# Kernel tuning notes

Measured on AMD Instinct MI355X. Metric: run time of the kernel, lower is better.

The kernel has to match this reference:

```python
import jax, jax.numpy as jnp
import numpy as np
from jax import lax

DIM = 384
HEADS = 8
H = W = 32
N = H * W
B = 8
FH, FW = 32, 17  # rfft2 spectral dims: H, W//2+1
EPS = 1e-5


def setup_inputs() -> dict:
    key = jax.random.key(0)
    ks = jax.random.split(key, 24)
    g = lambda i, shape, s=0.02: jax.random.normal(ks[i], shape, dtype=jnp.float32) * s
    inp = {
        "x": jax.random.normal(ks[0], (B, N, DIM), dtype=jnp.float32),
        "cw": g(1, (DIM, FH, FW, 2)),               # complex spectral weight
        # depthwise conv weights (C,1,3,3), kaiming-like std sqrt(2/(9))
        "dwq": jax.random.normal(ks[2], (DIM, 1, 3, 3), dtype=jnp.float32) * np.sqrt(2.0 / 9.0),
        "dwk": jax.random.normal(ks[3], (DIM, 1, 3, 3), dtype=jnp.float32) * np.sqrt(2.0 / 9.0),
        "dwv": jax.random.normal(ks[4], (DIM, 1, 3, 3), dtype=jnp.float32) * np.sqrt(2.0 / 9.0),
        # batchnorm params (inference mode)
        "gq": jnp.ones((DIM,), jnp.float32), "bq": jnp.zeros((DIM,), jnp.float32),
        "mq": g(5, (DIM,), 0.1), "vq": jnp.abs(g(6, (DIM,), 0.1)) + 1.0,
        "gk": jnp.ones((DIM,), jnp.float32), "bk": jnp.zeros((DIM,), jnp.float32),
        "mk": g(7, (DIM,), 0.1), "vk": jnp.abs(g(8, (DIM,), 0.1)) + 1.0,
        "gv": jnp.ones((DIM,), jnp.float32), "bv": jnp.zeros((DIM,), jnp.float32),
        "mv": g(9, (DIM,), 0.1), "vv": jnp.abs(g(10, (DIM,), 0.1)) + 1.0,
        # linear projections (torch Linear weight layout: (out,in), y = x @ W.T)
        "wq": g(11, (DIM, DIM)), "wk": g(12, (DIM, DIM)), "wv": g(13, (DIM, DIM)),
        "wo": g(14, (DIM, DIM)), "bo": jnp.zeros((DIM,), jnp.float32),
    }
    return inp


def _dw_bn(y, w, gamma, beta, mean, var):
    # depthwise 3x3 conv (stride 1, pad 1, no bias) + inference BN -> (B, N, C)
    y = lax.conv_general_dilated(
        y, w, window_strides=(1, 1), padding=[(1, 1), (1, 1)],
        dimension_numbers=("NCHW", "OIHW", "NCHW"), feature_group_count=DIM)
    scale = (gamma / jnp.sqrt(var + EPS))[None, :, None, None]
    shift = (beta - mean * gamma / jnp.sqrt(var + EPS))[None, :, None, None]
    y = y * scale + shift
    return y.reshape(y.shape[0], DIM, -1).transpose(0, 2, 1)  # b (h w) c


def reference(x, cw, dwq, dwk, dwv, gq, bq, mq, vq, gk, bk, mk, vk,
              gv, bv, mv, vv, wq, wk, wv, wo, bo):
    Bc, Nc, C = x.shape
    # --- F3Filter (flag='Learn'): FFT2 -> complex weight -> iFFT2 ---
    xi = x.reshape(Bc, H, W, C).transpose(0, 3, 1, 2)            # B,C,H,W
    xf = jnp.fft.rfft2(xi, axes=(2, 3), norm="ortho")            # B,C,H,W//2+1
    weight = cw[..., 0] + 1j * cw[..., 1]                        # C,FH,FW
    xr = jnp.fft.irfft2(xf * weight, s=(H, W), axes=(2, 3), norm="ortho")
    x_fft = xr.reshape(Bc, C, Nc).transpose(0, 2, 1)             # B,N,C

    # --- conv QKV projections on x_fft (as B,C,H,W = xr) ---
    q = _dw_bn(xr, dwq, gq, bq, mq, vq)
    k = _dw_bn(xr, dwk, gk, bk, mk, vk)
    v = _dw_bn(xr, dwv, gv, bv, mv, vv)

    hd = C // HEADS
    def split_heads(t):
        return t.reshape(Bc, Nc, HEADS, hd).transpose(0, 2, 1, 3)  # b h t d
    q = split_heads(q @ wq.T)
    k = split_heads(k @ wk.T)
    v = split_heads(v @ wv.T)

    scale = C ** (-0.5)  # note: full dim, as in the original
    attn = jax.nn.softmax(jnp.einsum("bhld,bhtd->bhlt", q, k) * scale, axis=-1)
    out = jnp.einsum("bhlt,bhtd->bhld", attn, v)
    out = out.transpose(0, 2, 1, 3).reshape(Bc, Nc, C)
    out = out @ wo.T + bo
    return x_fft + out
```

## Files before the change

kernel.cpp:

```cpp
#include <hip/hip_runtime.h>
#include <hip/hip_bf16.h>
#include <cmath>

#define CDIM 384
#define NB 8
#define NPIX 1024

typedef __attribute__((ext_vector_type(8))) short short8v;
typedef __attribute__((ext_vector_type(4))) float float4v;

__device__ __forceinline__ ushort f2bf(float f) {
  union { float f; unsigned u; } v; v.f = f;
  unsigned r = (v.u + 0x7fffu + ((v.u >> 16) & 1u)) >> 16;
  return (ushort)r;
}
__device__ __forceinline__ float bf2f(ushort u) {
  union { unsigned u; float f; } v; v.u = ((unsigned)u) << 16;
  return v.f;
}

__global__ __launch_bounds__(256) void prep_k(
    ushort* __restrict__ tbl,
    const float* __restrict__ wq, const float* __restrict__ wk,
    const float* __restrict__ wv, const float* __restrict__ wo,
    ushort* __restrict__ wqb, ushort* __restrict__ wkb,
    ushort* __restrict__ wvb, ushort* __restrict__ wob,
    const float* __restrict__ x, ushort* __restrict__ xc)
{
  __shared__ ushort T[128][33];
  if (blockIdx.x < 20) {
    int i = blockIdx.x * 256 + threadIdx.x;
    if (i >= 5 * 1024) return;
    int t = i >> 10, j = i & 1023, r = j >> 5, cidx = j & 31;
    float ang = (float)((r * cidx) & 31) * 0.19634954084936207f;
    float val;
    if (t == 0) val = cosf(ang);
    else if (t == 1) val = sinf(ang);
    else if (t == 2) val = -sinf(ang);
    else {
      if (cidx > 16) val = 0.f;
      else {
        float cv = (cidx == 0 || cidx == 16) ? 1.f : 2.f;
        val = (t == 3) ? cv * cosf(ang) : -cv * sinf(ang);
      }
    }
    tbl[i] = f2bf(val);
  } else if (blockIdx.x < 164) {
    int i = (blockIdx.x - 20) * 256 + threadIdx.x;
    if (i * 4 >= CDIM * CDIM) return;
    float4 va = *(const float4*)&wq[i * 4];
    float4 vb = *(const float4*)&wk[i * 4];
    float4 vc = *(const float4*)&wv[i * 4];
    float4 vd = *(const float4*)&wo[i * 4];
    ushort4 ra = { f2bf(va.x), f2bf(va.y), f2bf(va.z), f2bf(va.w) };
    ushort4 rb = { f2bf(vb.x), f2bf(vb.y), f2bf(vb.z), f2bf(vb.w) };
    ushort4 rc = { f2bf(vc.x), f2bf(vc.y), f2bf(vc.z), f2bf(vc.w) };
    ushort4 rd = { f2bf(vd.x), f2bf(vd.y), f2bf(vd.z), f2bf(vd.w) };
    *(ushort4*)&wqb[i * 4] = ra;
    *(ushort4*)&wkb[i * 4] = rb;
    *(ushort4*)&wvb[i * 4] = rc;
    *(ushort4*)&wob[i * 4] = rd;
  } else {
    int t = blockIdx.x - 164;
    int b = t / 96, rr = t % 96;
    int c0 = (rr >> 3) * 32, n0 = (rr & 7) * 128;
    for (int i = threadIdx.x; i < 4096; i += 256) {
      int n = i >> 5, c = i & 31;
      T[n][c] = f2bf(x[((long)(b * 1024 + n0 + n)) * CDIM + c0 + c]);
    }
    __syncthreads();
    for (int i = threadIdx.x; i < 4096; i += 256) {
      int c = i >> 7, n = i & 127;
      xc[((long)(b * CDIM + c0 + c)) * 1024 + n0 + n] = T[n][c];
    }
  }
}

__global__ __launch_bounds__(256) void fft_conv_k(
    const ushort* __restrict__ xc, const float* __restrict__ cw,
    const ushort* __restrict__ tbl,
    const float* __restrict__ dwq, const float* __restrict__ dwk, const float* __restrict__ dwv,
    const float* __restrict__ gq, const float* __restrict__ bq, const float* __restrict__ mq, const float* __restrict__ vq,
    const float* __restrict__ gk, const float* __restrict__ bk, const float* __restrict__ mk, const float* __restrict__ vk,
    const float* __restrict__ gv, const float* __restrict__ bv, const float* __restrict__ mv, const float* __restrict__ vv,
    ushort* __restrict__ yc,
    ushort* __restrict__ qc, ushort* __restrict__ kc, ushort* __restrict__ vc)
{
  const int b = blockIdx.x / CDIM, c = blockIdx.x % CDIM;
  const int tid = threadIdx.x;
  const int w = tid >> 6, lane = tid & 63;
  const int l15 = lane & 15, l16 = lane >> 4;
  __shared__ ushort B[11][32][40];
  __shared__ float Ysf[32][33];

  float wq9[9], wk9[9], wv9[9];
#pragma unroll
  for (int t = 0; t < 9; ++t) {
    wq9[t] = dwq[c * 9 + t];
    wk9[t] = dwk[c * 9 + t];
    wv9[t] = dwv[c * 9 + t];
  }
  float scq = gq[c] * rsqrtf(vq[c] + 1e-5f); float shq = bq[c] - mq[c] * scq;
  float sck = gk[c] * rsqrtf(vk[c] + 1e-5f); float shk = bk[c] - mk[c] * sck;
  float scv = gv[c] * rsqrtf(vv[c] + 1e-5f); float shv = bv[c] - mv[c] * scv;

  for (int i = tid; i < 640; i += 256) {
    int t = i >> 7, j = i & 127, r = j >> 2, s = j & 3;
    *(uint4*)&B[t][r][s * 8] = *(const uint4*)&tbl[t * 1024 + r * 32 + s * 8];
  }
  for (int i = tid; i < 1024; i += 256)
    B[5][i & 31][i >> 5] = xc[(long)(b * CDIM + c) * 1024 + i];
  __syncthreads();

  for (int j = w; j < 8; j += 4) {
    int o = j & 1, ut = (j >> 1) & 1, wt = (j >> 2) & 1;
    short8v af = *(const short8v*)&B[o == 0 ? 0 : 2][ut * 16 + l15][l16 * 8];
    short8v bf = *(const short8v*)&B[5][wt * 16 + l15][l16 * 8];
    float4v acc = {0.f, 0.f, 0.f, 0.f};
    acc = __builtin_amdgcn_mfma_f32_16x16x32_bf16(af, bf, acc, 0, 0, 0);
    int dst = (o == 0) ? 7 : 8;
#pragma unroll
    for (int r = 0; r < 4; ++r)
      B[dst][ut * 16 + l16 * 4 + r][wt * 16 + l15] = f2bf(acc[r]);
  }
  __syncthreads();

  for (int j = w; j < 8; j += 4) {
    int o = j & 1, ut = (j >> 1) & 1, vt = (j >> 2) & 1;
    short8v a1 = *(const short8v*)&B[o == 0 ? 7 : 8][ut * 16 + l15][l16 * 8];
    short8v b1 = *(const short8v*)&B[0][vt * 16 + l15][l16 * 8];
    short8v a2 = *(const short8v*)&B[o == 0 ? 8 : 7][ut * 16 + l15][l16 * 8];
    short8v b2 = *(const short8v*)&B[o == 0 ? 1 : 2][vt * 16 + l15][l16 * 8];
    float4v acc = {0.f, 0.f, 0.f, 0.f};
    acc = __builtin_amdgcn_mfma_f32_16x16x32_bf16(a1, b1, acc, 0, 0, 0);
    acc = __builtin_amdgcn_mfma_f32_16x16x32_bf16(a2, b2, acc, 0, 0, 0);
    int v = vt * 16 + l15;
    if (v < 17) {
      float* praw = (float*)&B[o == 0 ? 5 : 6][0][0];
#pragma unroll
      for (int r = 0; r < 4; ++r)
        praw[(ut * 16 + l16 * 4 + r) * 20 + v] = acc[r];
    }
  }
  __syncthreads();

  for (int i = tid; i < 150; i += 256) {
    int buf = i / 75, j2 = i % 75, r2 = 17 + j2 / 5, s2 = j2 % 5;
    uint4 z = {0u, 0u, 0u, 0u};
    *(uint4*)&B[9 + buf][r2][s2 * 8] = z;
  }
  {
    const float* xfr = (const float*)&B[5][0][0];
    const float* xfi = (const float*)&B[6][0][0];
    for (int e = tid; e < 544; e += 256) {
      int u = e / 17, v = e - u * 17;
      float fr = xfr[u * 20 + v], fi = xfi[u * 20 + v];
      float2 wc = *(const float2*)&cw[((long)(c * 32 + u) * 17 + v) * 2];
      B[9][v][u]  = f2bf(fr * wc.x - fi * wc.y);
      B[10][v][u] = f2bf(fr * wc.y + fi * wc.x);
    }
  }
  __syncthreads();

  for (int j = w; j < 8; j += 4) {
    int o = j & 1, ht = (j >> 1) & 1, vt = (j >> 2) & 1;
    short8v a1 = *(const short8v*)&B[0][ht * 16 + l15][l16 * 8];
    short8v b1 = *(const short8v*)&B[o == 0 ? 9 : 10][vt * 16 + l15][l16 * 8];
    short8v a2 = *(const short8v*)&B[o == 0 ? 2 : 1][ht * 16 + l15][l16 * 8];
    short8v b2 = *(const short8v*)&B[o == 0 ? 10 : 9][vt * 16 + l15][l16 * 8];
    float4v acc = {0.f, 0.f, 0.f, 0.f};
    acc = __builtin_amdgcn_mfma_f32_16x16x32_bf16(a1, b1, acc, 0, 0, 0);
    acc = __builtin_amdgcn_mfma_f32_16x16x32_bf16(a2, b2, acc, 0, 0, 0);
    int dst = (o == 0) ? 7 : 8;
#pragma unroll
    for (int r = 0; r < 4; ++r)
      B[dst][ht * 16 + l16 * 4 + r][vt * 16 + l15] = f2bf(acc[r]);
  }
  __syncthreads();

  {
    int ht = w & 1, wt = (w >> 1) & 1;
    short8v a1 = *(const short8v*)&B[7][ht * 16 + l15][l16 * 8];
    short8v b1 = *(const short8v*)&B[3][wt * 16 + l15][l16 * 8];
    short8v a2 = *(const short8v*)&B[8][ht * 16 + l15][l16 * 8];
    short8v b2 = *(const short8v*)&B[4][wt * 16 + l15][l16 * 8];
    float4v acc = {0.f, 0.f, 0.f, 0.f};
    acc = __builtin_amdgcn_mfma_f32_16x16x32_bf16(a1, b1, acc, 0, 0, 0);
    acc = __builtin_amdgcn_mfma_f32_16x16x32_bf16(a2, b2, acc, 0, 0, 0);
#pragma unroll
    for (int r = 0; r < 4; ++r) {
      int hh = ht * 16 + l16 * 4 + r, ww = wt * 16 + l15;
      float y = acc[r] * (1.0f / 1024.0f);
      Ysf[hh][ww] = y;
      yc[(long)(b * CDIM + c) * 1024 + hh * 32 + ww] = f2bf(y);
    }
  }
  __syncthreads();

  for (int i = tid; i < 1024; i += 256) {
    int hh = i >> 5, ww = i & 31;
    float aq = 0.f, ak = 0.f, av = 0.f;
#pragma unroll
    for (int dy = 0; dy < 3; ++dy) {
      int y0 = hh + dy - 1;
#pragma unroll
      for (int dx = 0; dx < 3; ++dx) {
        int x0 = ww + dx - 1;
        float xv = (y0 >= 0 && y0 < 32 && x0 >= 0 && x0 < 32) ? Ysf[y0][x0] : 0.f;
        int t = dy * 3 + dx;
        aq += xv * wq9[t]; ak += xv * wk9[t]; av += xv * wv9[t];
      }
    }
    long o = (long)(b * CDIM + c) * 1024 + i;
    qc[o] = f2bf(aq * scq + shq);
    kc[o] = f2bf(ak * sck + shk);
    vc[o] = f2bf(av * scv + shv);
  }
}

template<bool CMA>
__device__ __forceinline__ void gemm_body(
    const ushort* __restrict__ A, const ushort* __restrict__ Wb,
    const float* __restrict__ bias, const ushort* __restrict__ ycr,
    void* __restrict__ Cd, int flags, int bx, int by)
{
  __shared__ ushort As[128][72];
  __shared__ ushort Ws[64][72];
  const int tid = threadIdx.x;
  const int w = tid >> 6, lane = tid & 63;
  const int l15 = lane & 15, l16 = lane >> 4;
  const int wm = w >> 1, wn = w & 1;
  const int row0 = bx * 128, col0 = by * 64;
  const int btok = row0 >> 10;
  const int ntok0 = row0 & 1023;
  float4v acc[4][2];
#pragma unroll
  for (int i = 0; i < 4; ++i)
#pragma unroll
    for (int j = 0; j < 2; ++j) acc[i][j] = (float4v){0.f, 0.f, 0.f, 0.f};
  for (int kt = 0; kt < CDIM; kt += 64) {
    if (kt) __syncthreads();
    if (CMA) {
      const int g = tid & 15, u = tid >> 4;
      const int c0 = u * 4;
      const long abase = ((long)(btok * CDIM + kt + c0)) * 1024 + ntok0 + g * 8;
      uint4 t0 = *(const uint4*)&A[abase + 0 * 1024];
      uint4 t1 = *(const uint4*)&A[abase + 1 * 1024];
      uint4 t2 = *(const uint4*)&A[abase + 2 * 1024];
      uint4 t3 = *(const uint4*)&A[abase + 3 * 1024];
      const ushort* s0 = (const ushort*)&t0;
      const ushort* s1 = (const ushort*)&t1;
      const ushort* s2 = (const ushort*)&t2;
      const ushort* s3 = (const ushort*)&t3;
      const int colu = c0 ^ ((g & 7) << 3);
#pragma unroll
      for (int i = 0; i < 8; ++i) {
        uint2 wv;
        wv.x = (unsigned)s0[i] | ((unsigned)s1[i] << 16);
        wv.y = (unsigned)s2[i] | ((unsigned)s3[i] << 16);
        *(uint2*)&As[g * 8 + i][colu] = wv;
      }
    } else {
      for (int c = tid; c < 1024; c += 256) {
        int r = c >> 3, s = c & 7;
        *(uint4*)&As[r][s * 8] = *(const uint4*)&A[(long)(row0 + r) * CDIM + kt + s * 8];
      }
    }
    for (int c = tid; c < 512; c += 256) {
      int r = c >> 3, s = c & 7;
      *(uint4*)&Ws[r][s * 8] = *(const uint4*)&Wb[(long)(col0 + r) * CDIM + kt + s * 8];
    }
    __syncthreads();
#pragma unroll
    for (int s = 0; s < 2; ++s) {
      short8v a[4], bfr[2];
#pragma unroll
      for (int i = 0; i < 4; ++i) {
        int arow = wm * 64 + i * 16 + l15;
        int acol = s * 32 + l16 * 8;
        if (CMA) acol ^= (arow & 56);
        a[i] = *(const short8v*)&As[arow][acol];
      }
#pragma unroll
      for (int j = 0; j < 2; ++j)
        bfr[j] = *(const short8v*)&Ws[wn * 32 + j * 16 + l15][s * 32 + l16 * 8];
#pragma unroll
      for (int i = 0; i < 4; ++i)
#pragma unroll
        for (int j = 0; j < 2; ++j)
          acc[i][j] = __builtin_amdgcn_mfma_f32_16x16x32_bf16(a[i], bfr[j], acc[i][j], 0, 0, 0);
    }
  }
#pragma unroll
  for (int i = 0; i < 4; ++i)
#pragma unroll
    for (int j = 0; j < 2; ++j) {
      int col = col0 + wn * 32 + j * 16 + l15;
      int rbase = row0 + wm * 64 + i * 16 + l16 * 4;
      int ntok = ntok0 + wm * 64 + i * 16 + l16 * 4;
      if (flags == 2) {
        ushort4 pk = { f2bf(acc[i][j][0]), f2bf(acc[i][j][1]),
                       f2bf(acc[i][j][2]), f2bf(acc[i][j][3]) };
        *(ushort4*)&((ushort*)Cd)[((long)(btok * CDIM + col)) * 1024 + ntok] = pk;
      } else if (flags == 1) {
        ushort4 yv = *(const ushort4*)&ycr[((long)(btok * CDIM + col)) * 1024 + ntok];
        float bcol = bias[col];
        float* op = (float*)Cd;
        op[(long)(rbase + 0) * CDIM + col] = acc[i][j][0] + bcol + bf2f(yv.x);
        op[(long)(rbase + 1) * CDIM + col] = acc[i][j][1] + bcol + bf2f(yv.y);
        op[(long)(rbase + 2) * CDIM + col] = acc[i][j][2] + bcol + bf2f(yv.z);
        op[(long)(rbase + 3) * CDIM + col] = acc[i][j][3] + bcol + bf2f(yv.w);
      } else {
#pragma unroll
        for (int r = 0; r < 4; ++r)
          ((ushort*)Cd)[(long)(rbase + r) * CDIM + col] = f2bf(acc[i][j][r]);
      }
    }
}

__global__ __launch_bounds__(256) void gemm_qkv_k(
    const ushort* __restrict__ qc, const ushort* __restrict__ kc, const ushort* __restrict__ vc,
    const ushort* __restrict__ wqb, const ushort* __restrict__ wkb, const ushort* __restrict__ wvb,
    ushort* __restrict__ q1, ushort* __restrict__ k1, ushort* __restrict__ vtc)
{
  const int z = blockIdx.z;
  const ushort* A  = z == 0 ? qc  : z == 1 ? kc  : vc;
  const ushort* Wb = z == 0 ? wqb : z == 1 ? wkb : wvb;
  ushort*       C  = z == 0 ? q1  : z == 1 ? k1  : vtc;
  gemm_body<true>(A, Wb, nullptr, nullptr, C, z == 2 ? 2 : 0, blockIdx.x, blockIdx.y);
}

__global__ __launch_bounds__(256) void gemm_out_k(
    const ushort* __restrict__ A, const ushort* __restrict__ Wb,
    const float* __restrict__ bias, const ushort* __restrict__ ycr,
    float* __restrict__ Cd)
{
  gemm_body<false>(A, Wb, bias, ycr, Cd, 1, blockIdx.x, blockIdx.y);
}

__global__ __launch_bounds__(256) void attn_mfma_k(
    const ushort* __restrict__ q1, const ushort* __restrict__ k1,
    const ushort* __restrict__ vt, ushort* __restrict__ ao)
{
  const int bh = blockIdx.x, qt = blockIdx.y;
  const int b = bh >> 3, h = bh & 7;
  const int tid = threadIdx.x;
  const int w = tid >> 6, lane = tid & 63;
  const int l15 = lane & 15, l16 = lane >> 4;
  __shared__ ushort Ks[64][72], Vs[48][72], Ps[64][72];
  const float scale = 0.051031036307982884f;
  const long base = (long)b * NPIX * CDIM + h * 48;
  const long vbase = (long)bh * 48 * NPIX;

  const int i0 = tid, i1 = tid + 256, i2 = tid + 512;
  const int r0 = i0 / 6, s0 = i0 - r0 * 6;
  const ushort* gp0 = k1 + base + (long)r0 * CDIM + s0 * 8;
  const long st0 = (long)64 * CDIM;
  ushort* lp0 = &Ks[r0][s0 * 8];
  const ushort* gp1; long st1; ushort* lp1;
  if (i1 < 384) {
    int r = i1 / 6, s = i1 - r * 6;
    gp1 = k1 + base + (long)r * CDIM + s * 8; st1 = (long)64 * CDIM; lp1 = &Ks[r][s * 8];
  } else {
    int j = i1 - 384, d = j >> 3, s = j & 7;
    gp1 = vt + vbase + (long)d * NPIX + s * 8; st1 = 64; lp1 = &Vs[d][s * 8];
  }
  const int j2 = i2 - 384, d2 = j2 >> 3, s2 = j2 & 7;
  const ushort* gp2 = vt + vbase + (long)d2 * NPIX + s2 * 8;
  const long st2 = 64;
  ushort* lp2 = &Vs[d2][s2 * 8];

  if (tid < 128) {
    uint4 z4 = {0u, 0u, 0u, 0u};
    int r = tid >> 1, s = tid & 1;
    *(uint4*)&Ks[r][48 + s * 8] = z4;
  }
  const long qrow = base + (long)(qt * 64 + w * 16 + l15) * CDIM;
  short8v qa0 = *(const short8v*)&q1[qrow + l16 * 8];
  short8v qa1;
  {
    short8v qz = {};
    short8v qv = *(const short8v*)&q1[qrow + ((l16 < 2) ? 32 + l16 * 8 : 0)];
    qa1 = (l16 < 2) ? qv : qz;
  }

  float lrun[4] = {0.f, 0.f, 0.f, 0.f};
  float4v accO[3];
#pragma unroll
  for (int fd = 0; fd < 3; ++fd) accO[fd] = (float4v){0.f, 0.f, 0.f, 0.f};
  short8v onesb;
#pragma unroll
  for (int j = 0; j < 8; ++j) onesb[j] = (short)0x3F80;

  uint4 t0 = *(const uint4*)gp0;
  uint4 t1 = *(const uint4*)gp1;
  uint4 t2 = *(const uint4*)gp2;

  for (int kt = 0; kt < 16; ++kt) {
    *(uint4*)lp0 = t0;
    *(uint4*)lp1 = t1;
    *(uint4*)lp2 = t2;
    __syncthreads();
    if (kt + 1 < 16) {
      t0 = *(const uint4*)(gp0 + (long)(kt + 1) * st0);
      t1 = *(const uint4*)(gp1 + (long)(kt + 1) * st1);
      t2 = *(const uint4*)(gp2 + (long)(kt + 1) * st2);
    }
    float4v sacc[4];
#pragma unroll
    for (int fc = 0; fc < 4; ++fc) {
      short8v kb0 = *(const short8v*)&Ks[fc * 16 + l15][l16 * 8];
      short8v kb1 = *(const short8v*)&Ks[fc * 16 + l15][32 + l16 * 8];
      sacc[fc] = (float4v){0.f, 0.f, 0.f, 0.f};
      sacc[fc] = __builtin_amdgcn_mfma_f32_16x16x32_bf16(kb0, qa0, sacc[fc], 0, 0, 0);
      sacc[fc] = __builtin_amdgcn_mfma_f32_16x16x32_bf16(kb1, qa1, sacc[fc], 0, 0, 0);
    }
    unsigned* prow = (unsigned*)&Ps[w * 16 + l15][0];
#pragma unroll
    for (int fc = 0; fc < 4; ++fc) {
      float p0 = __expf(sacc[fc][0] * scale);
      float p1 = __expf(sacc[fc][1] * scale);
      float p2 = __expf(sacc[fc][2] * scale);
      float p3 = __expf(sacc[fc][3] * scale);
      __hip_bfloat162 d01 = __float22bfloat162_rn(make_float2(p0, p1));
      __hip_bfloat162 d23 = __float22bfloat162_rn(make_float2(p2, p3));
      prow[fc * 8 + l16 * 2 + 0] = *(unsigned*)&d01;
      prow[fc * 8 + l16 * 2 + 1] = *(unsigned*)&d23;
    }
    asm volatile("s_waitcnt lgkmcnt(0)" ::: "memory");
    __builtin_amdgcn_sched_barrier(0);
    short8v pa0 = *(const short8v*)&Ps[w * 16 + l15][l16 * 8];
    short8v pa1 = *(const short8v*)&Ps[w * 16 + l15][32 + l16 * 8];
    float4v srow = (float4v){0.f, 0.f, 0.f, 0.f};
    srow = __builtin_amdgcn_mfma_f32_16x16x32_bf16(pa0, onesb, srow, 0, 0, 0);
    srow = __builtin_amdgcn_mfma_f32_16x16x32_bf16(pa1, onesb, srow, 0, 0, 0);
#pragma unroll
    for (int r = 0; r < 4; ++r) lrun[r] += srow[r];
#pragma unroll
    for (int fd = 0; fd < 3; ++fd) {
      short8v vb0 = *(const short8v*)&Vs[fd * 16 + l15][l16 * 8];
      short8v vb1 = *(const short8v*)&Vs[fd * 16 + l15][32 + l16 * 8];
      accO[fd] = __builtin_amdgcn_mfma_f32_16x16x32_bf16(pa0, vb0, accO[fd], 0, 0, 0);
      accO[fd] = __builtin_amdgcn_mfma_f32_16x16x32_bf16(pa1, vb1, accO[fd], 0, 0, 0);
    }
    __syncthreads();
  }
  float inv[4];
#pragma unroll
  for (int r = 0; r < 4; ++r) inv[r] = 1.f / lrun[r];
#pragma unroll
  for (int fd = 0; fd < 3; ++fd)
#pragma unroll
    for (int r = 0; r < 4; ++r) {
      int qrow2 = qt * 64 + w * 16 + l16 * 4 + r;
      ao[base + (long)qrow2 * CDIM + fd * 16 + l15] = f2bf(accO[fd][r] * inv[r]);
    }
}

extern "C" void kernel_launch(void* const* d_in, const int* in_sizes, int n_in,
                              void* d_out, int out_size, void* d_ws, size_t ws_size,
                              hipStream_t stream) {
  const float* x   = (const float*)d_in[0];
  const float* cw  = (const float*)d_in[1];
  const float* dwq = (const float*)d_in[2];
  const float* dwk = (const float*)d_in[3];
  const float* dwv = (const float*)d_in[4];
  const float* gq  = (const float*)d_in[5];
  const float* bq  = (const float*)d_in[6];
  const float* mq  = (const float*)d_in[7];
  const float* vq  = (const float*)d_in[8];
  const float* gk  = (const float*)d_in[9];
  const float* bk  = (const float*)d_in[10];
  const float* mk  = (const float*)d_in[11];
  const float* vk  = (const float*)d_in[12];
  const float* gv  = (const float*)d_in[13];
  const float* bv  = (const float*)d_in[14];
  const float* mv  = (const float*)d_in[15];
  const float* vv  = (const float*)d_in[16];
  const float* wq  = (const float*)d_in[17];
  const float* wk  = (const float*)d_in[18];
  const float* wv  = (const float*)d_in[19];
  const float* wo  = (const float*)d_in[20];
  const float* bo  = (const float*)d_in[21];
  float* out = (float*)d_out;

  char* wsb = (char*)d_ws;
  const size_t H = (size_t)NB * NPIX * CDIM * 2;
  ushort* xcp = (ushort*)(wsb + 0 * H);
  ushort* vtc = (ushort*)(wsb + 0 * H);
  ushort* yc  = (ushort*)(wsb + 1 * H);
  ushort* qc  = (ushort*)(wsb + 2 * H);
  ushort* ao  = (ushort*)(wsb + 2 * H);
  ushort* kc  = (ushort*)(wsb + 3 * H);
  ushort* vc  = (ushort*)(wsb + 4 * H);
  ushort* q1  = (ushort*)(wsb + 5 * H);
  ushort* k1  = (ushort*)(wsb + 6 * H);
  ushort* wqb = (ushort*)(wsb + 7 * H);
  ushort* wkb = wqb + CDIM * CDIM;
  ushort* wvb = wkb + CDIM * CDIM;
  ushort* wob = wvb + CDIM * CDIM;
  ushort* tbl = wob + CDIM * CDIM;

  prep_k<<<dim3(932), 256, 0, stream>>>(tbl, wq, wk, wv, wo,
      wqb, wkb, wvb, wob, x, xcp);
  fft_conv_k<<<dim3(NB * CDIM), 256, 0, stream>>>(xcp, cw, tbl, dwq, dwk, dwv,
      gq, bq, mq, vq, gk, bk, mk, vk, gv, bv, mv, vv, yc, qc, kc, vc);
  gemm_qkv_k<<<dim3(64, 6, 3), 256, 0, stream>>>(qc, kc, vc, wqb, wkb, wvb, q1, k1, vtc);
  attn_mfma_k<<<dim3(64, 16), 256, 0, stream>>>(q1, k1, vtc, ao);
  gemm_out_k<<<dim3(64, 6), 256, 0, stream>>>(ao, wob, bo, yc, out);
}
```

Before: 103.3 us.

## Process two channels per FFT block and 128 query rows per attention block

The FFT/conv kernel now handles two channels per workgroup, halving the grid and sharing the DFT twiddle tables loaded into LDS, with depthwise and BN parameters read inline instead of hoisted. The attention kernel doubles its query tile to 128 rows so each K/V tile staged in LDS is reused for two row groups, halving K/V loads and block count. The cost is more LDS and registers per block, fewer blocks in flight, and possibly lower occupancy on the attention path.

```diff
diff --git a/kernel.cpp b/kernel.cpp
--- a/kernel.cpp
+++ b/kernel.cpp
@@ -86,57 +86,52 @@
     ushort* __restrict__ yc,
     ushort* __restrict__ qc, ushort* __restrict__ kc, ushort* __restrict__ vc)
 {
-  const int b = blockIdx.x / CDIM, c = blockIdx.x % CDIM;
+  const int bp = blockIdx.x;
+  const int b = bp / 192, cp = (bp % 192) * 2;
   const int tid = threadIdx.x;
   const int w = tid >> 6, lane = tid & 63;
   const int l15 = lane & 15, l16 = lane >> 4;
-  __shared__ ushort B[11][32][40];
-  __shared__ float Ysf[32][33];
-
-  float wq9[9], wk9[9], wv9[9];
-#pragma unroll
-  for (int t = 0; t < 9; ++t) {
-    wq9[t] = dwq[c * 9 + t];
-    wk9[t] = dwk[c * 9 + t];
-    wv9[t] = dwv[c * 9 + t];
-  }
-  float scq = gq[c] * rsqrtf(vq[c] + 1e-5f); float shq = bq[c] - mq[c] * scq;
-  float sck = gk[c] * rsqrtf(vk[c] + 1e-5f); float shk = bk[c] - mk[c] * sck;
-  float scv = gv[c] * rsqrtf(vv[c] + 1e-5f); float shv = bv[c] - mv[c] * scv;
+  __shared__ ushort Tb[5][32][40];
+  __shared__ ushort Wk[2][6][32][40];
+  __shared__ float Ysf[2][32][33];
 
   for (int i = tid; i < 640; i += 256) {
     int t = i >> 7, j = i & 127, r = j >> 2, s = j & 3;
-    *(uint4*)&B[t][r][s * 8] = *(const uint4*)&tbl[t * 1024 + r * 32 + s * 8];
-  }
-  for (int i = tid; i < 1024; i += 256)
-    B[5][i & 31][i >> 5] = xc[(long)(b * CDIM + c) * 1024 + i];
+    *(uint4*)&Tb[t][r][s * 8] = *(const uint4*)&tbl[t * 1024 + r * 32 + s * 8];
+  }
+  for (int i = tid; i < 2048; i += 256) {
+    int ch = i >> 10, idx = i & 1023;
+    Wk[ch][0][idx & 31][idx >> 5] = xc[(long)(b * CDIM + cp + ch) * 1024 + idx];
+  }
   __syncthreads();
 
-  for (int j = w; j < 8; j += 4) {
-    int o = j & 1, ut = (j >> 1) & 1, wt = (j >> 2) & 1;
-    short8v af = *(const short8v*)&B[o == 0 ? 0 : 2][ut * 16 + l15][l16 * 8];
-    short8v bf = *(const short8v*)&B[5][wt * 16 + l15][l16 * 8];
+  for (int j = w; j < 16; j += 4) {
+    int ch = j >> 3, jj = j & 7;
+    int o = jj & 1, ut = (jj >> 1) & 1, wt = (jj >> 2) & 1;
+    short8v af = *(const short8v*)&Tb[o == 0 ? 0 : 2][ut * 16 + l15][l16 * 8];
+    short8v bf = *(const short8v*)&Wk[ch][0][wt * 16 + l15][l16 * 8];
     float4v acc = {0.f, 0.f, 0.f, 0.f};
     acc = __builtin_amdgcn_mfma_f32_16x16x32_bf16(af, bf, acc, 0, 0, 0);
-    int dst = (o == 0) ? 7 : 8;
+    int dst = (o == 0) ? 2 : 3;
 #pragma unroll
     for (int r = 0; r < 4; ++r)
-      B[dst][ut * 16 + l16 * 4 + r][wt * 16 + l15] = f2bf(acc[r]);
+      Wk[ch][dst][ut * 16 + l16 * 4 + r][wt * 16 + l15] = f2bf(acc[r]);
   }
   __syncthreads();
 
-  for (int j = w; j < 8; j += 4) {
-    int o = j & 1, ut = (j >> 1) & 1, vt = (j >> 2) & 1;
-    short8v a1 = *(const short8v*)&B[o == 0 ? 7 : 8][ut * 16 + l15][l16 * 8];
-    short8v b1 = *(const short8v*)&B[0][vt * 16 + l15][l16 * 8];
-    short8v a2 = *(const short8v*)&B[o == 0 ? 8 : 7][ut * 16 + l15][l16 * 8];
-    short8v b2 = *(const short8v*)&B[o == 0 ? 1 : 2][vt * 16 + l15][l16 * 8];
+  for (int j = w; j < 16; j += 4) {
+    int ch = j >> 3, jj = j & 7;
+    int o = jj & 1, ut = (jj >> 1) & 1, vt = (jj >> 2) & 1;
+    short8v a1 = *(const short8v*)&Wk[ch][o == 0 ? 2 : 3][ut * 16 + l15][l16 * 8];
+    short8v b1 = *(const short8v*)&Tb[0][vt * 16 + l15][l16 * 8];
+    short8v a2 = *(const short8v*)&Wk[ch][o == 0 ? 3 : 2][ut * 16 + l15][l16 * 8];
+    short8v b2 = *(const short8v*)&Tb[o == 0 ? 1 : 2][vt * 16 + l15][l16 * 8];
     float4v acc = {0.f, 0.f, 0.f, 0.f};
     acc = __builtin_amdgcn_mfma_f32_16x16x32_bf16(a1, b1, acc, 0, 0, 0);
     acc = __builtin_amdgcn_mfma_f32_16x16x32_bf16(a2, b2, acc, 0, 0, 0);
     int v = vt * 16 + l15;
     if (v < 17) {
-      float* praw = (float*)&B[o == 0 ? 5 : 6][0][0];
+      float* praw = (float*)&Wk[ch][o == 0 ? 0 : 1][0][0];
 #pragma unroll
       for (int r = 0; r < 4; ++r)
         praw[(ut * 16 + l16 * 4 + r) * 20 + v] = acc[r];
@@ -144,46 +139,48 @@
   }
   __syncthreads();
 
-  for (int i = tid; i < 150; i += 256) {
-    int buf = i / 75, j2 = i % 75, r2 = 17 + j2 / 5, s2 = j2 % 5;
+  for (int i = tid; i < 300; i += 256) {
+    int ch = i / 150, j2 = i % 150;
+    int buf = j2 / 75, j3 = j2 % 75, r2 = 17 + j3 / 5, s2 = j3 % 5;
     uint4 z = {0u, 0u, 0u, 0u};
-    *(uint4*)&B[9 + buf][r2][s2 * 8] = z;
-  }
-  {
-    const float* xfr = (const float*)&B[5][0][0];
-    const float* xfi = (const float*)&B[6][0][0];
-    for (int e = tid; e < 544; e += 256) {
-      int u = e / 17, v = e - u * 17;
-      float fr = xfr[u * 20 + v], fi = xfi[u * 20 + v];
-      float2 wc = *(const float2*)&cw[((long)(c * 32 + u) * 17 + v) * 2];
-      B[9][v][u]  = f2bf(fr * wc.x - fi * wc.y);
-      B[10][v][u] = f2bf(fr * wc.y + fi * wc.x);
-    }
+    *(uint4*)&Wk[ch][4 + buf][r2][s2 * 8] = z;
+  }
+  for (int e = tid; e < 1088; e += 256) {
+    int ch = e >= 544 ? 1 : 0, e2 = e - ch * 544;
+    int u = e2 / 17, v = e2 - u * 17;
+    const float* xfr = (const float*)&Wk[ch][0][0][0];
+    const float* xfi = (const float*)&Wk[ch][1][0][0];
+    float fr = xfr[u * 20 + v], fi = xfi[u * 20 + v];
+    float2 wc = *(const float2*)&cw[((long)((cp + ch) * 32 + u) * 17 + v) * 2];
+    Wk[ch][4][v][u] = f2bf(fr * wc.x - fi * wc.y);
+    Wk[ch][5][v][u] = f2bf(fr * wc.y + fi * wc.x);
   }
   __syncthreads();
 
-  for (int j = w; j < 8; j += 4) {
-    int o = j & 1, ht = (j >> 1) & 1, vt = (j >> 2) & 1;
-    short8v a1 = *(const short8v*)&B[0][ht * 16 + l15][l16 * 8];
-    short8v b1 = *(const short8v*)&B[o == 0 ? 9 : 10][vt * 16 + l15][l16 * 8];
-    short8v a2 = *(const short8v*)&B[o == 0 ? 2 : 1][ht * 16 + l15][l16 * 8];
-    short8v b2 = *(const short8v*)&B[o == 0 ? 10 : 9][vt * 16 + l15][l16 * 8];
+  for (int j = w; j < 16; j += 4) {
+    int ch = j >> 3, jj = j & 7;
+    int o = jj & 1, ht = (jj >> 1) & 1, vt = (jj >> 2) & 1;
+    short8v a1 = *(const short8v*)&Tb[0][ht * 16 + l15][l16 * 8];
+    short8v b1 = *(const short8v*)&Wk[ch][o == 0 ? 4 : 5][vt * 16 + l15][l16 * 8];
+    short8v a2 = *(const short8v*)&Tb[o == 0 ? 2 : 1][ht * 16 + l15][l16 * 8];
+    short8v b2 = *(const short8v*)&Wk[ch][o == 0 ? 5 : 4][vt * 16 + l15][l16 * 8];
     float4v acc = {0.f, 0.f, 0.f, 0.f};
     acc = __builtin_amdgcn_mfma_f32_16x16x32_bf16(a1, b1, acc, 0, 0, 0);
     acc = __builtin_amdgcn_mfma_f32_16x16x32_bf16(a2, b2, acc, 0, 0, 0);
-    int dst = (o == 0) ? 7 : 8;
+    int dst = (o == 0) ? 2 : 3;
 #pragma unroll
     for (int r = 0; r < 4; ++r)
-      B[dst][ht * 16 + l16 * 4 + r][vt * 16 + l15] = f2bf(acc[r]);
+      Wk[ch][dst][ht * 16 + l16 * 4 + r][vt * 16 + l15] = f2bf(acc[r]);
   }
   __syncthreads();
 
-  {
-    int ht = w & 1, wt = (w >> 1) & 1;
-    short8v a1 = *(const short8v*)&B[7][ht * 16 + l15][l16 * 8];
-    short8v b1 = *(const short8v*)&B[3][wt * 16 + l15][l16 * 8];
-    short8v a2 = *(const short8v*)&B[8][ht * 16 + l15][l16 * 8];
-    short8v b2 = *(const short8v*)&B[4][wt * 16 + l15][l16 * 8];
+  for (int j = w; j < 8; j += 4) {
+    int ch = j >> 2, jj = j & 3;
+    int ht = jj & 1, wt = (jj >> 1) & 1;
+    short8v a1 = *(const short8v*)&Wk[ch][2][ht * 16 + l15][l16 * 8];
+    short8v b1 = *(const short8v*)&Tb[3][wt * 16 + l15][l16 * 8];
+    short8v a2 = *(const short8v*)&Wk[ch][3][ht * 16 + l15][l16 * 8];
+    short8v b2 = *(const short8v*)&Tb[4][wt * 16 + l15][l16 * 8];
     float4v acc = {0.f, 0.f, 0.f, 0.f};
     acc = __builtin_amdgcn_mfma_f32_16x16x32_bf16(a1, b1, acc, 0, 0, 0);
     acc = __builtin_amdgcn_mfma_f32_16x16x32_bf16(a2, b2, acc, 0, 0, 0);
@@ -191,14 +188,16 @@
     for (int r = 0; r < 4; ++r) {
       int hh = ht * 16 + l16 * 4 + r, ww = wt * 16 + l15;
       float y = acc[r] * (1.0f / 1024.0f);
-      Ysf[hh][ww] = y;
-      yc[(long)(b * CDIM + c) * 1024 + hh * 32 + ww] = f2bf(y);
+      Ysf[ch][hh][ww] = y;
+      yc[(long)(b * CDIM + cp + ch) * 1024 + hh * 32 + ww] = f2bf(y);
     }
   }
   __syncthreads();
 
-  for (int i = tid; i < 1024; i += 256) {
-    int hh = i >> 5, ww = i & 31;
+  for (int i = tid; i < 2048; i += 256) {
+    int ch = i >> 10, idx = i & 1023;
+    int c = cp + ch;
+    int hh = idx >> 5, ww = idx & 31;
     float aq = 0.f, ak = 0.f, av = 0.f;
 #pragma unroll
     for (int dy = 0; dy < 3; ++dy) {
@@ -206,15 +205,20 @@
 #pragma unroll
       for (int dx = 0; dx < 3; ++dx) {
         int x0 = ww + dx - 1;
-        float xv = (y0 >= 0 && y0 < 32 && x0 >= 0 && x0 < 32) ? Ysf[y0][x0] : 0.f;
+        float xv = (y0 >= 0 && y0 < 32 && x0 >= 0 && x0 < 32) ? Ysf[ch][y0][x0] : 0.f;
         int t = dy * 3 + dx;
-        aq += xv * wq9[t]; ak += xv * wk9[t]; av += xv * wv9[t];
+        aq += xv * dwq[c * 9 + t];
+        ak += xv * dwk[c * 9 + t];
+        av += xv * dwv[c * 9 + t];
       }
     }
-    long o = (long)(b * CDIM + c) * 1024 + i;
-    qc[o] = f2bf(aq * scq + shq);
-    kc[o] = f2bf(ak * sck + shk);
-    vc[o] = f2bf(av * scv + shv);
+    float scq = gq[c] * rsqrtf(vq[c] + 1e-5f);
+    float sck = gk[c] * rsqrtf(vk[c] + 1e-5f);
+    float scv = gv[c] * rsqrtf(vv[c] + 1e-5f);
+    long o = (long)(b * CDIM + c) * 1024 + idx;
+    qc[o] = f2bf(aq * scq + (bq[c] - mq[c] * scq));
+    kc[o] = f2bf(ak * sck + (bk[c] - mk[c] * sck));
+    vc[o] = f2bf(av * scv + (bv[c] - mv[c] * scv));
   }
 }
 
@@ -342,12 +346,12 @@
     const ushort* __restrict__ q1, const ushort* __restrict__ k1,
     const ushort* __restrict__ vt, ushort* __restrict__ ao)
 {
-  const int bh = blockIdx.x, qt = blockIdx.y;
+  const int bh = blockIdx.x, qt2 = blockIdx.y;
   const int b = bh >> 3, h = bh & 7;
   const int tid = threadIdx.x;
   const int w = tid >> 6, lane = tid & 63;
   const int l15 = lane & 15, l16 = lane >> 4;
-  __shared__ ushort Ks[64][72], Vs[48][72], Ps[64][72];
+  __shared__ ushort Ks[64][72], Vs[48][72], Ps[128][72];
   const float scale = 0.051031036307982884f;
   const long base = (long)b * NPIX * CDIM + h * 48;
   const long vbase = (long)bh * 48 * NPIX;
@@ -375,19 +379,26 @@
     int r = tid >> 1, s = tid & 1;
     *(uint4*)&Ks[r][48 + s * 8] = z4;
   }
-  const long qrow = base + (long)(qt * 64 + w * 16 + l15) * CDIM;
-  short8v qa0 = *(const short8v*)&q1[qrow + l16 * 8];
-  short8v qa1;
+  const long qrowA = base + (long)(qt2 * 128 + w * 16 + l15) * CDIM;
+  const long qrowB = qrowA + (long)64 * CDIM;
+  short8v qa0A = *(const short8v*)&q1[qrowA + l16 * 8];
+  short8v qa0B = *(const short8v*)&q1[qrowB + l16 * 8];
+  short8v qa1A, qa1B;
   {
     short8v qz = {};
-    short8v qv = *(const short8v*)&q1[qrow + ((l16 < 2) ? 32 + l16 * 8 : 0)];
-    qa1 = (l16 < 2) ? qv : qz;
-  }
-
-  float lrun[4] = {0.f, 0.f, 0.f, 0.f};
-  float4v accO[3];
-#pragma unroll
-  for (int fd = 0; fd < 3; ++fd) accO[fd] = (float4v){0.f, 0.f, 0.f, 0.f};
+    short8v qvA = *(const short8v*)&q1[qrowA + ((l16 < 2) ? 32 + l16 * 8 : 0)];
+    short8v qvB = *(const short8v*)&q1[qrowB + ((l16 < 2) ? 32 + l16 * 8 : 0)];
+    qa1A = (l16 < 2) ? qvA : qz;
+    qa1B = (l16 < 2) ? qvB : qz;
+  }
+
+  float lrunA[4] = {0.f, 0.f, 0.f, 0.f}, lrunB[4] = {0.f, 0.f, 0.f, 0.f};
+  float4v accOA[3], accOB[3];
+#pragma unroll
+  for (int fd = 0; fd < 3; ++fd) {
+    accOA[fd] = (float4v){0.f, 0.f, 0.f, 0.f};
+    accOB[fd] = (float4v){0.f, 0.f, 0.f, 0.f};
+  }
   short8v onesb;
 #pragma unroll
   for (int j = 0; j < 8; ++j) onesb[j] = (short)0x3F80;
@@ -406,54 +417,70 @@
       t1 = *(const uint4*)(gp1 + (long)(kt + 1) * st1);
       t2 = *(const uint4*)(gp2 + (long)(kt + 1) * st2);
     }
-    float4v sacc[4];
+    float4v saccA[4], saccB[4];
 #pragma unroll
     for (int fc = 0; fc < 4; ++fc) {
       short8v kb0 = *(const short8v*)&Ks[fc * 16 + l15][l16 * 8];
       short8v kb1 = *(const short8v*)&Ks[fc * 16 + l15][32 + l16 * 8];
-      sacc[fc] = (float4v){0.f, 0.f, 0.f, 0.f};
-      sacc[fc] = __builtin_amdgcn_mfma_f32_16x16x32_bf16(kb0, qa0, sacc[fc], 0, 0, 0);
-      sacc[fc] = __builtin_amdgcn_mfma_f32_16x16x32_bf16(kb1, qa1, sacc[fc], 0, 0, 0);
-    }
-    unsigned* prow = (unsigned*)&Ps[w * 16 + l15][0];
+      saccA[fc] = (float4v){0.f, 0.f, 0.f, 0.f};
+      saccA[fc] = __builtin_amdgcn_mfma_f32_16x16x32_bf16(kb0, qa0A, saccA[fc], 0, 0, 0);
+      saccA[fc] = __builtin_amdgcn_mfma_f32_16x16x32_bf16(kb1, qa1A, saccA[fc], 0, 0, 0);
+      saccB[fc] = (float4v){0.f, 0.f, 0.f, 0.f};
+      saccB[fc] = __builtin_amdgcn_mfma_f32_16x16x32_bf16(kb0, qa0B, saccB[fc], 0, 0, 0);
+      saccB[fc] = __builtin_amdgcn_mfma_f32_16x16x32_bf16(kb1, qa1B, saccB[fc], 0, 0, 0);
+    }
+    unsigned* prowA = (unsigned*)&Ps[w * 16 + l15][0];
+    unsigned* prowB = (unsigned*)&Ps[64 + w * 16 + l15][0];
 #pragma unroll
     for (int fc = 0; fc < 4; ++fc) {
-      float p0 = __expf(sacc[fc][0] * scale);
-      float p1 = __expf(sacc[fc][1] * scale);
-      float p2 = __expf(sacc[fc][2] * scale);
-      float p3 = __expf(sacc[fc][3] * scale);
-      __hip_bfloat162 d01 = __float22bfloat162_rn(make_float2(p0, p1));
-      __hip_bfloat162 d23 = __float22bfloat162_rn(make_float2(p2, p3));
-      prow[fc * 8 + l16 * 2 + 0] = *(unsigned*)&d01;
-      prow[fc * 8 + l16 * 2 + 1] = *(unsigned*)&d23;
+      float a0 = __expf(saccA[fc][0] * scale), a1 = __expf(saccA[fc][1] * scale);
+      float a2 = __expf(saccA[fc][2] * scale), a3 = __expf(saccA[fc][3] * scale);
+      __hip_bfloat162 dA01 = __float22bfloat162_rn(make_float2(a0, a1));
+      __hip_bfloat162 dA23 = __float22bfloat162_rn(make_float2(a2, a3));
+      prowA[fc * 8 + l16 * 2 + 0] = *(unsigned*)&dA01;
+      prowA[fc * 8 + l16 * 2 + 1] = *(unsigned*)&dA23;
+      float b0 = __expf(saccB[fc][0] * scale), b1 = __expf(saccB[fc][1] * scale);
+      float b2 = __expf(saccB[fc][2] * scale), b3 = __expf(saccB[fc][3] * scale);
+      __hip_bfloat162 dB01 = __float22bfloat162_rn(make_float2(b0, b1));
+      __hip_bfloat162 dB23 = __float22bfloat162_rn(make_float2(b2, b3));
+      prowB[fc * 8 + l16 * 2 + 0] = *(unsigned*)&dB01;
+      prowB[fc * 8 + l16 * 2 + 1] = *(unsigned*)&dB23;
     }
     asm volatile("s_waitcnt lgkmcnt(0)" ::: "memory");
     __builtin_amdgcn_sched_barrier(0);
-    short8v pa0 = *(const short8v*)&Ps[w * 16 + l15][l16 * 8];
-    short8v pa1 = *(const short8v*)&Ps[w * 16 + l15][32 + l16 * 8];
-    float4v srow = (float4v){0.f, 0.f, 0.f, 0.f};
-    srow = __builtin_amdgcn_mfma_f32_16x16x32_bf16(pa0, onesb, srow, 0, 0, 0);
-    srow = __builtin_amdgcn_mfma_f32_16x16x32_bf16(pa1, onesb, srow, 0, 0, 0);
-#pragma unroll
-    for (int r = 0; r < 4; ++r) lrun[r] += srow[r];
+    short8v pa0A = *(const short8v*)&Ps[w * 16 + l15][l16 * 8];
+    short8v pa1A = *(const short8v*)&Ps[w * 16 + l15][32 + l16 * 8];
+    short8v pa0B = *(const short8v*)&Ps[64 + w * 16 + l15][l16 * 8];
+    short8v pa1B = *(const short8v*)&Ps[64 + w * 16 + l15][32 + l16 * 8];
+    float4v srA = (float4v){0.f, 0.f, 0.f, 0.f};
+    srA = __builtin_amdgcn_mfma_f32_16x16x32_bf16(pa0A, onesb, srA, 0, 0, 0);
+    srA = __builtin_amdgcn_mfma_f32_16x16x32_bf16(pa1A, onesb, srA, 0, 0, 0);
+    float4v srB = (float4v){0.f, 0.f, 0.f, 0.f};
+    srB = __builtin_amdgcn_mfma_f32_16x16x32_bf16(pa0B, onesb, srB, 0, 0, 0);
+    srB = __builtin_amdgcn_mfma_f32_16x16x32_bf16(pa1B, onesb, srB, 0, 0, 0);
+#pragma unroll
+    for (int r = 0; r < 4; ++r) { lrunA[r] += srA[r]; lrunB[r] += srB[r]; }
 #pragma unroll
     for (int fd = 0; fd < 3; ++fd) {
       short8v vb0 = *(const short8v*)&Vs[fd * 16 + l15][l16 * 8];
       short8v vb1 = *(const short8v*)&Vs[fd * 16 + l15][32 + l16 * 8];
-      accO[fd] = __builtin_amdgcn_mfma_f32_16x16x32_bf16(pa0, vb0, accO[fd], 0, 0, 0);
-      accO[fd] = __builtin_amdgcn_mfma_f32_16x16x32_bf16(pa1, vb1, accO[fd], 0, 0, 0);
+      accOA[fd] = __builtin_amdgcn_mfma_f32_16x16x32_bf16(pa0A, vb0, accOA[fd], 0, 0, 0);
+      accOA[fd] = __builtin_amdgcn_mfma_f32_16x16x32_bf16(pa1A, vb1, accOA[fd], 0, 0, 0);
+      accOB[fd] = __builtin_amdgcn_mfma_f32_16x16x32_bf16(pa0B, vb0, accOB[fd], 0, 0, 0);
+      accOB[fd] = __builtin_amdgcn_mfma_f32_16x16x32_bf16(pa1B, vb1, accOB[fd], 0, 0, 0);
     }
     __syncthreads();
   }
-  float inv[4];
-#pragma unroll
-  for (int r = 0; r < 4; ++r) inv[r] = 1.f / lrun[r];
+  float invA[4], invB[4];
+#pragma unroll
+  for (int r = 0; r < 4; ++r) { invA[r] = 1.f / lrunA[r]; invB[r] = 1.f / lrunB[r]; }
 #pragma unroll
   for (int fd = 0; fd < 3; ++fd)
 #pragma unroll
     for (int r = 0; r < 4; ++r) {
-      int qrow2 = qt * 64 + w * 16 + l16 * 4 + r;
-      ao[base + (long)qrow2 * CDIM + fd * 16 + l15] = f2bf(accO[fd][r] * inv[r]);
+      int qrA = qt2 * 128 + w * 16 + l16 * 4 + r;
+      ao[base + (long)qrA * CDIM + fd * 16 + l15] = f2bf(accOA[fd][r] * invA[r]);
+      ao[base + (long)(qrA + 64) * CDIM + fd * 16 + l15] = f2bf(accOB[fd][r] * invB[r]);
     }
 }
 
@@ -503,9 +530,9 @@
 
   prep_k<<<dim3(932), 256, 0, stream>>>(tbl, wq, wk, wv, wo,
       wqb, wkb, wvb, wob, x, xcp);
-  fft_conv_k<<<dim3(NB * CDIM), 256, 0, stream>>>(xcp, cw, tbl, dwq, dwk, dwv,
+  fft_conv_k<<<dim3(NB * CDIM / 2), 256, 0, stream>>>(xcp, cw, tbl, dwq, dwk, dwv,
       gq, bq, mq, vq, gk, bk, mk, vk, gv, bv, mv, vv, yc, qc, kc, vc);
   gemm_qkv_k<<<dim3(64, 6, 3), 256, 0, stream>>>(qc, kc, vc, wqb, wkb, wvb, q1, k1, vtc);
-  attn_mfma_k<<<dim3(64, 16), 256, 0, stream>>>(q1, k1, vtc, ao);
+  attn_mfma_k<<<dim3(64, 8), 256, 0, stream>>>(q1, k1, vtc, ao);
   gemm_out_k<<<dim3(64, 6), 256, 0, stream>>>(ao, wob, bo, yc, out);
 }
```

New measurement: 112.2 us. +8.7%, slower.
